# Performance work log

Measured on AMD Instinct MI355X. Metric: run time of the kernel, lower is better.

The kernel has to match this reference:

```python
import jax, jax.numpy as jnp
import numpy as np

N_NODES = 50000


def _gcn_conv(x, edge_index, W, b):
    # PyG GCNConv (default flags): add self-loops, symmetric normalization,
    # linear transform, scatter-add aggregation, bias.
    N = x.shape[0]
    row, col = edge_index[0], edge_index[1]  # messages flow row -> col
    loop = jnp.arange(N)
    row_f = jnp.concatenate([row, loop])
    col_f = jnp.concatenate([col, loop])
    deg = jax.ops.segment_sum(jnp.ones(col_f.shape[0], dtype=x.dtype), col_f,
                              num_segments=N)
    deg_inv_sqrt = jnp.where(deg > 0, jax.lax.rsqrt(jnp.maximum(deg, 1e-12)), 0.0)
    norm = deg_inv_sqrt[row_f] * deg_inv_sqrt[col_f]  # [E+N]
    h = x @ W                                          # [N, out]
    msg = h[row_f] * norm[:, None]                     # gather + scale
    out = jax.ops.segment_sum(msg, col_f, num_segments=N)  # scatter-add
    return out + b


def setup_inputs() -> dict:
    key = jax.random.key(0)
    ks = jax.random.split(key, 6)
    d_in, d_hid, d_out = 128, 128, 64
    E = 800000
    x = jax.random.normal(ks[0], (N_NODES, d_in), dtype=jnp.float32)
    edge_index = jax.random.randint(ks[1], (2, E), 0, N_NODES, dtype=jnp.int64)
    edge_label = jax.random.uniform(ks[2], (100000,), dtype=jnp.float32)
    edge_label_index = jax.random.randint(ks[3], (2, 100000), 0, N_NODES,
                                          dtype=jnp.int64)
    # Glorot-style init for GCNConv linear weights
    W1 = jax.random.normal(ks[4], (d_in, d_hid), dtype=jnp.float32) / np.sqrt(d_in)
    b1 = jnp.zeros((d_hid,), dtype=jnp.float32)
    W2 = jax.random.normal(ks[5], (d_hid, d_out), dtype=jnp.float32) / np.sqrt(d_hid)
    b2 = jnp.zeros((d_out,), dtype=jnp.float32)
    return {"x": x, "edge_index": edge_index, "edge_label": edge_label,
            "edge_label_index": edge_label_index,
            "W1": W1, "b1": b1, "W2": W2, "b2": b2}


def reference(x, edge_index, edge_label, edge_label_index, W1, b1, W2, b2):
    h = jax.nn.relu(_gcn_conv(x, edge_index, W1, b1))
    # dropout is identity in eval mode (training=False)
    z = _gcn_conv(h, edge_index, W2, b2)
    return z
```

## Files before the change

kernel.cpp:

```cpp
#include <hip/hip_runtime.h>


typedef unsigned int u32;
typedef unsigned short ushort;
typedef __attribute__((ext_vector_type(8))) short short8;
typedef __attribute__((ext_vector_type(8))) unsigned short us8;
typedef __attribute__((ext_vector_type(4))) float floatx4;

static inline int cdiv_l(long a, int b) { return (int)((a + b - 1) / b); }

constexpr int NPB  = 256;
constexpr int EPB  = 4096;
constexpr int MAXB = 256;
constexpr int CAP  = 8192;

__device__ __forceinline__ u32 pack_bf16(float a, float b) {
  union { float f; u32 i; } ua, ub;
  ua.f = a; ub.f = b;
  u32 x = (ua.i + 0x7fffu + ((ua.i >> 16) & 1u)) >> 16;
  u32 y = (ub.i + 0x7fffu + ((ub.i >> 16) & 1u)) & 0xffff0000u;
  return x | y;
}

__device__ __forceinline__ short bf16r(float f) {
  union { float f; u32 i; } u; u.f = f;
  return (short)((u.i + 0x7fffu + ((u.i >> 16) & 1u)) >> 16);
}

__device__ __forceinline__ void dq8(float* a, uint2 v, float sd) {
  a[0] += (float)(v.x & 255u) * sd;
  a[1] += (float)((v.x >> 8) & 255u) * sd;
  a[2] += (float)((v.x >> 16) & 255u) * sd;
  a[3] += (float)(v.x >> 24) * sd;
  a[4] += (float)(v.y & 255u) * sd;
  a[5] += (float)((v.y >> 8) & 255u) * sd;
  a[6] += (float)((v.y >> 16) & 255u) * sd;
  a[7] += (float)(v.y >> 24) * sd;
}

__global__ __launch_bounds__(256) void k_pack(
    const float* __restrict__ W1, const float* __restrict__ W2,
    u32* __restrict__ w1f, u32* __restrict__ w2f, int* __restrict__ cur) {
  const int tid = threadIdx.x;
  const int b = blockIdx.x;
  if (b == 0 && tid < MAXB) cur[tid] = 0;
  if (b < 8) {
    const int s = b * 256 + tid;
    const int lane = s & 63, frag = s >> 6;
    const int kc = frag >> 3, cb = frag & 7;
    const float* src =
        W1 + (long)(kc * 32 + (lane >> 4) * 8) * 128 + cb * 16 + (lane & 15);
    u32 o[4];
#pragma unroll
    for (int p = 0; p < 4; ++p)
      o[p] = pack_bf16(src[(2 * p) * 128], src[(2 * p + 1) * 128]);
    *(uint4*)(w1f + (long)s * 4) = make_uint4(o[0], o[1], o[2], o[3]);
  } else {
    const int s = (b - 8) * 256 + tid;
    const int lane = s & 63, frag = s >> 6;
    const int kc = frag >> 2, cb = frag & 3;
    const float* src =
        W2 + (long)(kc * 32 + (lane >> 4) * 8) * 64 + cb * 16 + (lane & 15);
    u32 o[4];
#pragma unroll
    for (int p = 0; p < 4; ++p)
      o[p] = pack_bf16(src[(2 * p) * 64], src[(2 * p + 1) * 64]);
    *(uint4*)(w2f + (long)s * 4) = make_uint4(o[0], o[1], o[2], o[3]);
  }
}

__global__ __launch_bounds__(256) void k_fused1(
    const int* __restrict__ ei, int* __restrict__ cur, u32* __restrict__ ebuf,
    int E, int NBE,
    const float* __restrict__ x, const u32* __restrict__ w1f,
    u32* __restrict__ h8, float* __restrict__ scale, int N) {
  __shared__ float eb[4][16 * 133];
  const int tid = threadIdx.x;

  if (blockIdx.x < (unsigned)NBE) {
    u32* ecache = (u32*)&eb[0][0];
    int* hist   = (int*)&eb[2][0];
    int* curs   = hist + MAXB;
    const int* ecol = ei + E;
    if (tid < MAXB) hist[tid] = 0;
    __syncthreads();
    const int base = blockIdx.x * EPB;
#pragma unroll
    for (int j = 0; j < EPB / 256; ++j) {
      int e = base + j * 256 + tid;
      u32 pk = 0xffffffffu;
      if (e < E) {
        u32 r = (u32)ei[e];
        u32 c = (u32)ecol[e];
        pk = r | (c << 16);
        atomicAdd(hist + (c >> 8), 1);
      }
      ecache[j * 256 + tid] = pk;
    }
    __syncthreads();
    if (tid < MAXB) {
      int n = hist[tid];
      curs[tid] = tid * CAP + (n ? atomicAdd(cur + tid, n) : 0);
    }
    __syncthreads();
#pragma unroll
    for (int j = 0; j < EPB / 256; ++j) {
      u32 pk = ecache[j * 256 + tid];
      if (pk != 0xffffffffu) {
        u32 c = pk >> 16;
        int b = c >> 8;
        int p = atomicAdd(curs + b, 1);
        if (p < (b + 1) * CAP)
          ebuf[p] = (pk & 0xffffu) | ((c & (NPB - 1)) << 16);
      }
    }
    return;
  }

  constexpr int K = 128, NC = 8, LROW = 133;
  const int w = tid >> 6, lane = tid & 63;
  const int quad = lane >> 4, n16 = lane & 15;
  const int row0 = ((blockIdx.x - NBE) * 4 + w) * 16;

  floatx4 acc[NC];
#pragma unroll
  for (int c = 0; c < NC; ++c) acc[c] = {0.f, 0.f, 0.f, 0.f};

  const int am = row0 + n16;
  const bool av = am < N;
  const float* arow = x + (long)am * K;
  const short8* wf = (const short8*)w1f;

#pragma unroll
  for (int kc = 0; kc < 4; ++kc) {
    const int kb = kc * 32 + quad * 8;
    float4 a0 = make_float4(0.f, 0.f, 0.f, 0.f);
    float4 a1 = make_float4(0.f, 0.f, 0.f, 0.f);
    if (av) {
      a0 = *(const float4*)(arow + kb);
      a1 = *(const float4*)(arow + kb + 4);
    }
    short8 af;
    af[0] = bf16r(a0.x); af[1] = bf16r(a0.y); af[2] = bf16r(a0.z); af[3] = bf16r(a0.w);
    af[4] = bf16r(a1.x); af[5] = bf16r(a1.y); af[6] = bf16r(a1.z); af[7] = bf16r(a1.w);
#pragma unroll
    for (int c = 0; c < NC; ++c) {
      short8 bf = wf[(kc * 8 + c) * 64 + lane];
      acc[c] = __builtin_amdgcn_mfma_f32_16x16x32_bf16(af, bf, acc[c], 0, 0, 0);
    }
  }

  float* ep = eb[w];
#pragma unroll
  for (int c = 0; c < NC; ++c)
#pragma unroll
    for (int r = 0; r < 4; ++r)
      ep[(quad * 4 + r) * LROW + c * 16 + n16] = acc[c][r];
  __syncthreads();

  const int rr = lane >> 2, seg = lane & 3;
  const float* rowp = ep + rr * LROW + seg * 32;
  float m = 0.f;
#pragma unroll
  for (int c = 0; c < 32; ++c) m = fmaxf(m, fabsf(rowp[c]));
  m = fmaxf(m, __shfl_xor(m, 1, 4));
  m = fmaxf(m, __shfl_xor(m, 2, 4));
  const float inv = (m > 0.f) ? 127.f / m : 0.f;
  const float s = m / 127.f;
  u32 q[8];
#pragma unroll
  for (int wd = 0; wd < 8; ++wd) {
    u32 b0 = (u32)((int)rintf(rowp[wd * 4 + 0] * inv) + 128);
    u32 b1 = (u32)((int)rintf(rowp[wd * 4 + 1] * inv) + 128);
    u32 b2 = (u32)((int)rintf(rowp[wd * 4 + 2] * inv) + 128);
    u32 b3 = (u32)((int)rintf(rowp[wd * 4 + 3] * inv) + 128);
    q[wd] = (b0 & 255u) | ((b1 & 255u) << 8) | ((b2 & 255u) << 16) | (b3 << 24);
  }
  const int rg = row0 + rr;
  if (rg < N) {
    uint4* dst = (uint4*)(h8 + (long)rg * 32 + seg * 8);
    dst[0] = make_uint4(q[0], q[1], q[2], q[3]);
    dst[1] = make_uint4(q[4], q[5], q[6], q[7]);
    if (seg == 0) scale[rg] = s;
  }
}

__global__ __launch_bounds__(1024) void k_csr(const u32* __restrict__ ebuf,
                                              const int* __restrict__ cur,
                                              const float* __restrict__ scale,
                                              int* __restrict__ off,
                                              int* __restrict__ deg,
                                              float* __restrict__ dis,
                                              float* __restrict__ sd,
                                              ushort* __restrict__ csr, int N) {
  __shared__ u32 ecache[CAP];
  __shared__ int cnt[NPB];
  __shared__ int curl[NPB];
  __shared__ int wsum[NPB / 64];
  const int tid = threadIdx.x;
  const int b = blockIdx.x;
  const int s = b * CAP;
  const int e = s + min(cur[b], CAP);
  if (tid < NPB) cnt[tid] = 0;
  __syncthreads();
  for (int i = s + tid; i < e; i += 1024) {
    u32 pk = ebuf[i];
    ecache[i - s] = pk;
    atomicAdd(cnt + (pk >> 16), 1);
  }
  __syncthreads();
  const int lane = tid & 63, w = tid >> 6;
  int v = 0, vp = 0, incl = 0;
  if (tid < NPB) {
    v = cnt[tid];
    vp = (v + 7) & ~7;
    incl = vp;
#pragma unroll
    for (int d = 1; d < 64; d <<= 1) {
      int x = __shfl_up(incl, d, 64);
      if (lane >= d) incl += x;
    }
    if (lane == 63) wsum[w] = incl;
  }
  __syncthreads();
  if (w == 0 && lane < NPB / 64) {
    int sv = wsum[lane];
#pragma unroll
    for (int d = 1; d < NPB / 64; d <<= 1) {
      int x = __shfl_up(sv, d, 64);
      if (lane >= d) sv += x;
    }
    wsum[lane] = sv;
  }
  __syncthreads();
  if (tid < NPB) {
    const int excl = ((w > 0) ? wsum[w - 1] : 0) + incl - vp;
    const int node = b * NPB + tid;
    if (node < N) {
      float dv = rsqrtf((float)v + 1.0f);
      off[node] = s + excl;
      deg[node] = v;
      dis[node] = dv;
      sd[node] = scale[node] * dv;
    }
    curl[tid] = excl;
  }
  __syncthreads();
  for (int i = s + tid; i < e; i += 1024) {
    u32 pk = ecache[i - s];
    int p = atomicAdd(curl + (pk >> 16), 1);
    csr[s + p] = (ushort)(pk & 0xffffu);
  }
}

__global__ __launch_bounds__(256) void k_gg(
    const uint2* __restrict__ h8, const int* __restrict__ off,
    const int* __restrict__ deg, const ushort* __restrict__ csr,
    const float* __restrict__ dis, const float* __restrict__ sd,
    const float* __restrict__ b1, const u32* __restrict__ w2f,
    u32* __restrict__ h2, float* __restrict__ s2, int N) {
  constexpr int LG = 65;
  constexpr int LC = 66;
  __shared__ u32 lg[16 * LG];
  __shared__ float cb[16 * LC];
  const int tid = threadIdx.x;
  const int r = tid >> 4;
  const int lf = tid & 15;
  const int row0 = blockIdx.x * 16;
  const int n = row0 + r;

  u32 gw[4] = {0, 0, 0, 0};
  if (n < N) {
    const int s = off[n], e = s + deg[n];
    const float dn = dis[n];
    float acc[8] = {};
    float K = 0.f;
    {
      float sn = sd[n];
      dq8(acc, h8[(long)n * 16 + lf], sn);
      K += sn;
    }
    int j = s;
    for (; j + 8 <= e; j += 8) {
      us8 ev = *(const us8*)(csr + j);
      const int i0 = ev[0], i1 = ev[1], i2 = ev[2], i3 = ev[3];
      const int i4 = ev[4], i5 = ev[5], i6 = ev[6], i7 = ev[7];
      const float d0 = sd[i0], d1 = sd[i1], d2 = sd[i2], d3 = sd[i3];
      const float d4 = sd[i4], d5 = sd[i5], d6 = sd[i6], d7 = sd[i7];
      uint2 v0 = h8[(long)i0 * 16 + lf];
      uint2 v1 = h8[(long)i1 * 16 + lf];
      uint2 v2 = h8[(long)i2 * 16 + lf];
      uint2 v3 = h8[(long)i3 * 16 + lf];
      uint2 v4 = h8[(long)i4 * 16 + lf];
      uint2 v5 = h8[(long)i5 * 16 + lf];
      uint2 v6 = h8[(long)i6 * 16 + lf];
      uint2 v7 = h8[(long)i7 * 16 + lf];
      dq8(acc, v0, d0); dq8(acc, v1, d1); dq8(acc, v2, d2); dq8(acc, v3, d3);
      dq8(acc, v4, d4); dq8(acc, v5, d5); dq8(acc, v6, d6); dq8(acc, v7, d7);
      K += ((d0 + d1) + (d2 + d3)) + ((d4 + d5) + (d6 + d7));
    }
    if (j < e) {
      us8 ev = *(const us8*)(csr + j);
#pragma unroll
      for (int t = 0; t < 8; ++t) {
        if (j + t < e) {
          const int it = ev[t];
          const float dt = sd[it];
          dq8(acc, h8[(long)it * 16 + lf], dt);
          K += dt;
        }
      }
    }
    const int f8 = lf * 8;
    const float4 bv0 = *(const float4*)(b1 + f8);
    const float4 bv1 = *(const float4*)(b1 + f8 + 4);
    const float bb[8] = {bv0.x, bv0.y, bv0.z, bv0.w, bv1.x, bv1.y, bv1.z, bv1.w};
    const float kc = 128.f * K;
#pragma unroll
    for (int q = 0; q < 8; ++q)
      acc[q] = fmaxf((acc[q] - kc) * dn + bb[q], 0.f);
#pragma unroll
    for (int q = 0; q < 4; ++q)
      gw[q] = pack_bf16(acc[2 * q], acc[2 * q + 1]);
  }
#pragma unroll
  for (int q = 0; q < 4; ++q) lg[r * LG + lf * 4 + q] = gw[q];
  __syncthreads();

  const int w = tid >> 6, lane = tid & 63;
  const int quad = lane >> 4, n16 = lane & 15;
  floatx4 acc4 = {0.f, 0.f, 0.f, 0.f};
#pragma unroll
  for (int kc = 0; kc < 4; ++kc) {
    const int kb = kc * 32 + quad * 8;
    const u32* ap = &lg[n16 * LG + (kb >> 1)];
    u32 aw[4] = {ap[0], ap[1], ap[2], ap[3]};
    short8 af = *(short8*)aw;
    short8 bf = ((const short8*)w2f)[(kc * 4 + w) * 64 + lane];
    acc4 = __builtin_amdgcn_mfma_f32_16x16x32_bf16(af, bf, acc4, 0, 0, 0);
  }
  float dd[4];
#pragma unroll
  for (int r4 = 0; r4 < 4; ++r4) {
    int rg = row0 + quad * 4 + r4;
    dd[r4] = (rg < N) ? dis[rg] : 0.f;
  }
#pragma unroll
  for (int r4 = 0; r4 < 4; ++r4)
    cb[(quad * 4 + r4) * LC + w * 16 + n16] = acc4[r4] * dd[r4];
  __syncthreads();

  const int rr2 = tid >> 4, lf2 = tid & 15;
  const float* rp = cb + rr2 * LC + lf2 * 4;
  float mx = fmaxf(fmaxf(fabsf(rp[0]), fabsf(rp[1])),
                   fmaxf(fabsf(rp[2]), fabsf(rp[3])));
  mx = fmaxf(mx, __shfl_xor(mx, 1, 16));
  mx = fmaxf(mx, __shfl_xor(mx, 2, 16));
  mx = fmaxf(mx, __shfl_xor(mx, 4, 16));
  mx = fmaxf(mx, __shfl_xor(mx, 8, 16));
  const float inv2 = (mx > 0.f) ? 127.f / mx : 0.f;
  const int rg2 = row0 + rr2;
  if (rg2 < N) {
    u32 q0 = (u32)((int)rintf(rp[0] * inv2) + 128);
    u32 q1 = (u32)((int)rintf(rp[1] * inv2) + 128);
    u32 q2 = (u32)((int)rintf(rp[2] * inv2) + 128);
    u32 q3 = (u32)((int)rintf(rp[3] * inv2) + 128);
    h2[(long)rg2 * 16 + lf2] =
        (q0 & 255u) | ((q1 & 255u) << 8) | ((q2 & 255u) << 16) | (q3 << 24);
    if (lf2 == 0) s2[rg2] = mx / 127.f;
  }
}

__global__ __launch_bounds__(256) void k_gather2(
    const uint2* __restrict__ hs, const int* __restrict__ off,
    const int* __restrict__ deg, const ushort* __restrict__ csr,
    const float* __restrict__ dis, const float* __restrict__ sc2,
    const float* __restrict__ bias, float* __restrict__ out, int N) {
  constexpr int L = 8;
  const int local = threadIdx.x / L;
  const int lf = threadIdx.x % L;
  const int n = blockIdx.x * (256 / L) + local;
  if (n >= N) return;
  const int s = off[n], e = s + deg[n];
  float acc[8] = {};
  float K = 0.f;
  {
    float t0 = sc2[n];
    dq8(acc, hs[(long)n * L + lf], t0);
    K += t0;
  }
  int j = s;
  for (; j + 8 <= e; j += 8) {
    us8 ev = *(const us8*)(csr + j);
    const int i0 = ev[0], i1 = ev[1], i2 = ev[2], i3 = ev[3];
    const int i4 = ev[4], i5 = ev[5], i6 = ev[6], i7 = ev[7];
    const float d0 = sc2[i0], d1 = sc2[i1], d2 = sc2[i2], d3 = sc2[i3];
    const float d4 = sc2[i4], d5 = sc2[i5], d6 = sc2[i6], d7 = sc2[i7];
    uint2 v0 = hs[(long)i0 * L + lf];
    uint2 v1 = hs[(long)i1 * L + lf];
    uint2 v2 = hs[(long)i2 * L + lf];
    uint2 v3 = hs[(long)i3 * L + lf];
    uint2 v4 = hs[(long)i4 * L + lf];
    uint2 v5 = hs[(long)i5 * L + lf];
    uint2 v6 = hs[(long)i6 * L + lf];
    uint2 v7 = hs[(long)i7 * L + lf];
    dq8(acc, v0, d0); dq8(acc, v1, d1); dq8(acc, v2, d2); dq8(acc, v3, d3);
    dq8(acc, v4, d4); dq8(acc, v5, d5); dq8(acc, v6, d6); dq8(acc, v7, d7);
    K += ((d0 + d1) + (d2 + d3)) + ((d4 + d5) + (d6 + d7));
  }
  if (j < e) {
    us8 ev = *(const us8*)(csr + j);
#pragma unroll
    for (int t = 0; t < 8; ++t) {
      if (j + t < e) {
        const int it = ev[t];
        const float dt = sc2[it];
        dq8(acc, hs[(long)it * L + lf], dt);
        K += dt;
      }
    }
  }
  const float d = dis[n];
  const float kc = 128.f * K;
  const int f8 = lf * 8;
  const float4 b0 = *(const float4*)(bias + f8);
  const float4 b1v = *(const float4*)(bias + f8 + 4);
  float4 o0, o1;
  o0.x = (acc[0] - kc) * d + b0.x;
  o0.y = (acc[1] - kc) * d + b0.y;
  o0.z = (acc[2] - kc) * d + b0.z;
  o0.w = (acc[3] - kc) * d + b0.w;
  o1.x = (acc[4] - kc) * d + b1v.x;
  o1.y = (acc[5] - kc) * d + b1v.y;
  o1.z = (acc[6] - kc) * d + b1v.z;
  o1.w = (acc[7] - kc) * d + b1v.w;
  *(float4*)(out + (long)n * 64 + f8) = o0;
  *(float4*)(out + (long)n * 64 + f8 + 4) = o1;
}

extern "C" void kernel_launch(void* const* d_in, const int* in_sizes, int n_in,
                              void* d_out, int out_size, void* d_ws, size_t ws_size,
                              hipStream_t stream) {
  const float* x  = (const float*)d_in[0];
  const int*   ei = (const int*)d_in[1];
  const float* W1 = (const float*)d_in[4];
  const float* b1 = (const float*)d_in[5];
  const float* W2 = (const float*)d_in[6];
  const float* b2 = (const float*)d_in[7];
  float* out = (float*)d_out;

  const int N = in_sizes[0] / 128;
  const int E = in_sizes[1] / 2;
  const int NBKT = cdiv_l(N, NPB);
  const int NBE  = cdiv_l(E, EPB);
  const int G1   = cdiv_l(N, 64);

  const long Np = (N + 64) & ~63L;
  const long BW = (long)NBKT * CAP;
  int*    cur   = (int*)d_ws;
  int*    off   = cur + 256;
  int*    deg   = off + Np;
  float*  dis   = (float*)(deg + Np);
  float*  scale = dis + Np;
  float*  sd    = scale + Np;
  float*  s2    = sd + Np;
  u32*    w1f   = (u32*)(s2 + Np);
  u32*    w2f   = w1f + 8192;
  u32*    ebuf  = w2f + 4096;
  ushort* csr   = (ushort*)(ebuf + BW);
  u32*    h8    = (u32*)(csr + BW);
  u32*    h2    = h8 + (long)N * 32;

  k_pack<<<12, 256, 0, stream>>>(W1, W2, w1f, w2f, cur);

  k_fused1<<<NBE + G1, 256, 0, stream>>>(ei, cur, ebuf, E, NBE, x, w1f, h8,
                                         scale, N);

  k_csr<<<NBKT, 1024, 0, stream>>>(ebuf, cur, scale, off, deg, dis, sd, csr, N);

  k_gg<<<cdiv_l(N, 16), 256, 0, stream>>>((const uint2*)h8, off, deg, csr,
                                          dis, sd, b1, w2f, h2, s2, N);

  k_gather2<<<cdiv_l(N, 32), 256, 0, stream>>>((const uint2*)h2, off, deg, csr,
                                               dis, s2, b2, out, N);
}
```

Baseline: 147.3 us.

## Replace global-atomic edge bucketing with per-block local sort and prefix offsets

Each edge block now sorts its edges by destination bucket in shared memory and writes them contiguously to its own slice of the global buffer, publishing an inclusive per-bucket prefix array in place of global atomic cursors. The CSR kernel then reads each block's run for its bucket using those prefixes and gathers them into shared memory before the count and scatter steps. This removes the global atomics and the scattered global writes, and drops the cursor reset from the pack kernel. In exchange it adds extra scans and reads of many short runs with only 4 threads per run, which may give poorly coalesced loads.

```diff
diff --git a/kernel.cpp b/kernel.cpp
--- a/kernel.cpp
+++ b/kernel.cpp
@@ -40,10 +40,9 @@
 
 __global__ __launch_bounds__(256) void k_pack(
     const float* __restrict__ W1, const float* __restrict__ W2,
-    u32* __restrict__ w1f, u32* __restrict__ w2f, int* __restrict__ cur) {
+    u32* __restrict__ w1f, u32* __restrict__ w2f) {
   const int tid = threadIdx.x;
   const int b = blockIdx.x;
-  if (b == 0 && tid < MAXB) cur[tid] = 0;
   if (b < 8) {
     const int s = b * 256 + tid;
     const int lane = s & 63, frag = s >> 6;
@@ -70,19 +69,21 @@
 }
 
 __global__ __launch_bounds__(256) void k_fused1(
-    const int* __restrict__ ei, int* __restrict__ cur, u32* __restrict__ ebuf,
-    int E, int NBE,
+    const int* __restrict__ ei, u32* __restrict__ ebuf,
+    int* __restrict__ inclg, int E, int NBE,
     const float* __restrict__ x, const u32* __restrict__ w1f,
     u32* __restrict__ h8, float* __restrict__ scale, int N) {
-  __shared__ float eb[4][16 * 133];
+  __shared__ __align__(16) char smem[35072];
   const int tid = threadIdx.x;
 
   if (blockIdx.x < (unsigned)NBE) {
-    u32* ecache = (u32*)&eb[0][0];
-    int* hist   = (int*)&eb[2][0];
-    int* curs   = hist + MAXB;
+    u32* ecache = (u32*)smem;
+    u32* sorted = ecache + EPB;
+    int* hist   = (int*)(sorted + EPB);
+    int* pexcl  = hist + MAXB;
+    int* wsum4  = pexcl + MAXB;
     const int* ecol = ei + E;
-    if (tid < MAXB) hist[tid] = 0;
+    hist[tid] = 0;
     __syncthreads();
     const int base = blockIdx.x * EPB;
 #pragma unroll
@@ -98,22 +99,43 @@
       ecache[j * 256 + tid] = pk;
     }
     __syncthreads();
-    if (tid < MAXB) {
-      int n = hist[tid];
-      curs[tid] = tid * CAP + (n ? atomicAdd(cur + tid, n) : 0);
-    }
+    const int lane = tid & 63, w = tid >> 6;
+    const int v = hist[tid];
+    int incl = v;
+#pragma unroll
+    for (int d = 1; d < 64; d <<= 1) {
+      int xx = __shfl_up(incl, d, 64);
+      if (lane >= d) incl += xx;
+    }
+    if (lane == 63) wsum4[w] = incl;
+    __syncthreads();
+    if (w == 0 && lane < 4) {
+      int sv = wsum4[lane];
+#pragma unroll
+      for (int d = 1; d < 4; d <<= 1) {
+        int xx = __shfl_up(sv, d, 64);
+        if (lane >= d) sv += xx;
+      }
+      wsum4[lane] = sv;
+    }
+    __syncthreads();
+    const int excl = ((w > 0) ? wsum4[w - 1] : 0) + incl - v;
+    inclg[blockIdx.x * MAXB + tid] = excl + v;
+    pexcl[tid] = excl;
     __syncthreads();
 #pragma unroll
     for (int j = 0; j < EPB / 256; ++j) {
       u32 pk = ecache[j * 256 + tid];
       if (pk != 0xffffffffu) {
-        u32 c = pk >> 16;
-        int b = c >> 8;
-        int p = atomicAdd(curs + b, 1);
-        if (p < (b + 1) * CAP)
-          ebuf[p] = (pk & 0xffffu) | ((c & (NPB - 1)) << 16);
+        u32 c16 = pk >> 16;
+        int p = atomicAdd(pexcl + (c16 >> 8), 1);
+        sorted[p] = (pk & 0xffffu) | ((c16 & 255u) << 16);
       }
     }
+    __syncthreads();
+    const int tot = pexcl[MAXB - 1];
+    u32* gout = ebuf + (long)blockIdx.x * EPB;
+    for (int i = tid; i < tot; i += 256) gout[i] = sorted[i];
     return;
   }
 
@@ -150,7 +172,7 @@
     }
   }
 
-  float* ep = eb[w];
+  float* ep = (float*)smem + w * (16 * LROW);
 #pragma unroll
   for (int c = 0; c < NC; ++c)
 #pragma unroll
@@ -186,30 +208,84 @@
 }
 
 __global__ __launch_bounds__(1024) void k_csr(const u32* __restrict__ ebuf,
-                                              const int* __restrict__ cur,
+                                              const int* __restrict__ inclg,
                                               const float* __restrict__ scale,
                                               int* __restrict__ off,
                                               int* __restrict__ deg,
                                               float* __restrict__ dis,
                                               float* __restrict__ sd,
-                                              ushort* __restrict__ csr, int N) {
+                                              ushort* __restrict__ csr,
+                                              int NBE, int N) {
   __shared__ u32 ecache[CAP];
+  __shared__ int rs[256], rl[256], gp[256];
   __shared__ int cnt[NPB];
   __shared__ int curl[NPB];
-  __shared__ int wsum[NPB / 64];
+  __shared__ int wsum[4];
+  __shared__ int tot_s;
   const int tid = threadIdx.x;
   const int b = blockIdx.x;
-  const int s = b * CAP;
-  const int e = s + min(cur[b], CAP);
-  if (tid < NPB) cnt[tid] = 0;
-  __syncthreads();
-  for (int i = s + tid; i < e; i += 1024) {
-    u32 pk = ebuf[i];
-    ecache[i - s] = pk;
-    atomicAdd(cnt + (pk >> 16), 1);
-  }
-  __syncthreads();
   const int lane = tid & 63, w = tid >> 6;
+
+  if (tid < 256) {
+    if (tid < NBE) {
+      int inc = inclg[tid * MAXB + b];
+      int prev = (b > 0) ? inclg[tid * MAXB + b - 1] : 0;
+      rs[tid] = prev;
+      rl[tid] = inc - prev;
+    } else {
+      rs[tid] = 0; rl[tid] = 0;
+    }
+    cnt[tid] = 0;
+  }
+  __syncthreads();
+  if (tid < 256) {
+    const int rv = rl[tid];
+    int rincl = rv;
+#pragma unroll
+    for (int d = 1; d < 64; d <<= 1) {
+      int xx = __shfl_up(rincl, d, 64);
+      if (lane >= d) rincl += xx;
+    }
+    if (lane == 63) wsum[w] = rincl;
+  }
+  __syncthreads();
+  if (w == 0 && lane < 4) {
+    int sv = wsum[lane];
+#pragma unroll
+    for (int d = 1; d < 4; d <<= 1) {
+      int xx = __shfl_up(sv, d, 64);
+      if (lane >= d) sv += xx;
+    }
+    wsum[lane] = sv;
+  }
+  __syncthreads();
+  if (tid < 256) {
+    const int rv = rl[tid];
+    int rincl = rv;
+#pragma unroll
+    for (int d = 1; d < 64; d <<= 1) {
+      int xx = __shfl_up(rincl, d, 64);
+      if (lane >= d) rincl += xx;
+    }
+    gp[tid] = ((w > 0) ? wsum[w - 1] : 0) + rincl - rv;
+    if (tid == 255) tot_s = gp[255] + rv;
+  }
+  __syncthreads();
+  const int tot = min(tot_s, CAP);
+  {
+    const int c4 = tid;
+    if (c4 < NBE * 4) {
+      const int c = c4 >> 2, j = c4 & 3;
+      const long src = (long)c * EPB + rs[c];
+      const int len = rl[c], g0 = gp[c];
+      for (int k = j; k < len; k += 4)
+        if (g0 + k < CAP) ecache[g0 + k] = ebuf[src + k];
+    }
+  }
+  __syncthreads();
+  for (int i = tid; i < tot; i += 1024)
+    atomicAdd(cnt + (ecache[i] >> 16), 1);
+  __syncthreads();
   int v = 0, vp = 0, incl = 0;
   if (tid < NPB) {
     v = cnt[tid];
@@ -217,8 +293,8 @@
     incl = vp;
 #pragma unroll
     for (int d = 1; d < 64; d <<= 1) {
-      int x = __shfl_up(incl, d, 64);
-      if (lane >= d) incl += x;
+      int xx = __shfl_up(incl, d, 64);
+      if (lane >= d) incl += xx;
     }
     if (lane == 63) wsum[w] = incl;
   }
@@ -227,8 +303,8 @@
     int sv = wsum[lane];
 #pragma unroll
     for (int d = 1; d < NPB / 64; d <<= 1) {
-      int x = __shfl_up(sv, d, 64);
-      if (lane >= d) sv += x;
+      int xx = __shfl_up(sv, d, 64);
+      if (lane >= d) sv += xx;
     }
     wsum[lane] = sv;
   }
@@ -238,7 +314,7 @@
     const int node = b * NPB + tid;
     if (node < N) {
       float dv = rsqrtf((float)v + 1.0f);
-      off[node] = s + excl;
+      off[node] = b * CAP + excl;
       deg[node] = v;
       dis[node] = dv;
       sd[node] = scale[node] * dv;
@@ -246,10 +322,11 @@
     curl[tid] = excl;
   }
   __syncthreads();
-  for (int i = s + tid; i < e; i += 1024) {
-    u32 pk = ecache[i - s];
+  ushort* cw = csr + (long)b * CAP;
+  for (int i = tid; i < tot; i += 1024) {
+    u32 pk = ecache[i];
     int p = atomicAdd(curl + (pk >> 16), 1);
-    csr[s + p] = (ushort)(pk & 0xffffu);
+    cw[p] = (ushort)(pk & 0xffffu);
   }
 }
 
@@ -456,9 +533,8 @@
   const int G1   = cdiv_l(N, 64);
 
   const long Np = (N + 64) & ~63L;
-  const long BW = (long)NBKT * CAP;
-  int*    cur   = (int*)d_ws;
-  int*    off   = cur + 256;
+  int*    inclg = (int*)d_ws;
+  int*    off   = inclg + (long)NBE * MAXB;
   int*    deg   = off + Np;
   float*  dis   = (float*)(deg + Np);
   float*  scale = dis + Np;
@@ -467,16 +543,17 @@
   u32*    w1f   = (u32*)(s2 + Np);
   u32*    w2f   = w1f + 8192;
   u32*    ebuf  = w2f + 4096;
-  ushort* csr   = (ushort*)(ebuf + BW);
-  u32*    h8    = (u32*)(csr + BW);
+  ushort* csr   = (ushort*)(ebuf + (long)NBE * EPB);
+  u32*    h8    = (u32*)(csr + (long)NBKT * CAP);
   u32*    h2    = h8 + (long)N * 32;
 
-  k_pack<<<12, 256, 0, stream>>>(W1, W2, w1f, w2f, cur);
-
-  k_fused1<<<NBE + G1, 256, 0, stream>>>(ei, cur, ebuf, E, NBE, x, w1f, h8,
+  k_pack<<<12, 256, 0, stream>>>(W1, W2, w1f, w2f);
+
+  k_fused1<<<NBE + G1, 256, 0, stream>>>(ei, ebuf, inclg, E, NBE, x, w1f, h8,
                                          scale, N);
 
-  k_csr<<<NBKT, 1024, 0, stream>>>(ebuf, cur, scale, off, deg, dis, sd, csr, N);
+  k_csr<<<NBKT, 1024, 0, stream>>>(ebuf, inclg, scale, off, deg, dis, sd, csr,
+                                   NBE, N);
 
   k_gg<<<cdiv_l(N, 16), 256, 0, stream>>>((const uint2*)h8, off, deg, csr,
                                           dis, sd, b1, w2f, h2, s2, N);
```

Result: no change. 147.6 us (+0.2%).
